# Performance work log

Hardware: AMD Instinct MI355X
Metric: run time of the kernel (lower is better)

The kernel has to match this reference:

```python
import jax, jax.numpy as jnp
import numpy as np

B, N, M, D = 8, 4096, 4096, 3


def setup_inputs() -> dict:
    key = jax.random.key(0)
    k1, k2 = jax.random.split(key)
    preds = jax.random.normal(k1, (B, M, D), dtype=jnp.float32)
    gts = jax.random.normal(k2, (B, N, D), dtype=jnp.float32)
    c = jnp.ones((1,), dtype=jnp.float32)
    return {"preds": preds, "gts": gts, "c": c}


def _huber(x, c):
    return jnp.where(x < c, 0.5 * x * x, c * x - 0.5 * c * c)


def reference(preds, gts, c):
    # P[b, i, j] = ||gts[b,i] - preds[b,j]||^2  (as in batch_pairwise_dist(gts, preds))
    rx = jnp.sum(gts * gts, axis=-1)              # [B, N]
    ry = jnp.sum(preds * preds, axis=-1)          # [B, M]
    zz = jnp.einsum('bnd,bmd->bnm', gts, preds)   # [B, N, M]
    P = rx[:, :, None] + ry[:, None, :] - 2.0 * zz
    mins1 = jnp.min(P, axis=1)                    # [B, M] min over gts
    mins2 = jnp.min(P, axis=2)                    # [B, N] min over preds
    loss = jnp.sum(_huber(mins1, c)) + jnp.sum(_huber(mins2, c))
    return loss
```

## Files before the change

kernel.cpp:

```cpp
#include <hip/hip_runtime.h>

typedef float v2f  __attribute__((ext_vector_type(2)));
typedef float v4f  __attribute__((ext_vector_type(4)));

#define NPTS   4096
#define NB     8
#define NZ     16
#define QPT    8
#define TPB    256
#define QPB    (TPB * QPT)
#define XB     (NPTS / QPB)
#define CHUNK  128
#define NGRP   (CHUNK / 4)
#define NCHUNK (NPTS / CHUNK)

__device__ __forceinline__ unsigned enc_f(float f) {
    unsigned u = __float_as_uint(f);
    return (u & 0x80000000u) ? ~u : (u | 0x80000000u);
}
__device__ __forceinline__ float dec_f(unsigned e) {
    unsigned u = (e & 0x80000000u) ? (e ^ 0x80000000u) : ~e;
    return __uint_as_float(u);
}

__device__ __forceinline__ v2f pk_fma(v2f a, v2f b, v2f c) {
    v2f d;
    asm("v_pk_fma_f32 %0, %1, %2, %3" : "=v"(d) : "v"(a), "v"(b), "v"(c));
    return d;
}
__device__ __forceinline__ v2f pk_mul(v2f a, v2f b) {
    v2f d;
    asm("v_pk_mul_f32 %0, %1, %2" : "=v"(d) : "v"(a), "v"(b));
    return d;
}
__device__ __forceinline__ float min3f(float a, float b, float c) {
    float d;
    asm("v_min3_f32 %0, %1, %2, %3" : "=v"(d) : "v"(a), "v"(b), "v"(c));
    return d;
}

__global__ __launch_bounds__(TPB, 2) void min_kernel(const float* __restrict__ preds,
                                                     const float* __restrict__ gts,
                                                     unsigned* __restrict__ mins) {
    const int z    = blockIdx.z;
    const int b    = z >> 1;
    const int pass = z & 1;
    const int tid  = threadIdx.x;

    const float* pts = pass ? preds : gts;
    const float* qrs = pass ? gts   : preds;

    __shared__ v4f SX[NGRP], SY[NGRP], SZ[NGRP];

    {
        const float* pb = pts + ((size_t)b * NPTS + blockIdx.y * CHUNK) * 3;
        if (tid < CHUNK) {
            ((float*)SX)[tid] = pb[tid * 3 + 0];
            ((float*)SY)[tid] = pb[tid * 3 + 1];
            ((float*)SZ)[tid] = pb[tid * 3 + 2];
        }
    }

    const float* qb    = qrs + (size_t)b * NPTS * 3;
    const int    jbase = blockIdx.x * QPB + tid;
    v2f   AX[QPT], AY[QPT], AZ[QPT];
    float R[QPT], acc[QPT];
#pragma unroll
    for (int q = 0; q < QPT; ++q) {
        int   j  = jbase + q * TPB;
        float qx = qb[j * 3 + 0];
        float qy = qb[j * 3 + 1];
        float qz = qb[j * 3 + 2];
        R[q]  = fmaf(qx, qx, fmaf(qy, qy, qz * qz));
        float ax = -2.0f * qx, ay = -2.0f * qy, az = -2.0f * qz;
        AX[q] = (v2f){ax, ax};
        AY[q] = (v2f){ay, ay};
        AZ[q] = (v2f){az, az};
        acc[q] = 3.4e38f;
    }
    __syncthreads();

#pragma unroll 2
    for (int g = 0; g < NGRP; ++g) {
        v4f X = SX[g], Y = SY[g], Z = SZ[g];
        v2f Xlo = X.lo, Xhi = X.hi;
        v2f Ylo = Y.lo, Yhi = Y.hi;
        v2f Zlo = Z.lo, Zhi = Z.hi;
        v2f Wlo = pk_fma(Xlo, Xlo, pk_fma(Ylo, Ylo, pk_mul(Zlo, Zlo)));
        v2f Whi = pk_fma(Xhi, Xhi, pk_fma(Yhi, Yhi, pk_mul(Zhi, Zhi)));
#pragma unroll
        for (int q = 0; q < QPT; ++q) {
            v2f t0 = pk_fma(Xlo, AX[q], pk_fma(Ylo, AY[q], pk_fma(Zlo, AZ[q], Wlo)));
            v2f t1 = pk_fma(Xhi, AX[q], pk_fma(Yhi, AY[q], pk_fma(Zhi, AZ[q], Whi)));
            acc[q] = min3f(t0.x, t0.y, min3f(t1.x, t1.y, acc[q]));
        }
    }

    unsigned* mz = mins + (size_t)z * NPTS;
#pragma unroll
    for (int q = 0; q < QPT; ++q) {
        atomicMin(&mz[jbase + q * TPB], enc_f(R[q] + acc[q]));
    }
}

__global__ __launch_bounds__(1024) void huberfinal_kernel(const unsigned* __restrict__ mins,
                                                          const float* __restrict__ cp,
                                                          float* __restrict__ out) {
    const float c = cp[0];
    float acc = 0.0f;
#pragma unroll 4
    for (int i = threadIdx.x; i < NZ * NPTS; i += 1024) {
        float x = dec_f(mins[i]);
        acc += (x < c) ? (0.5f * x * x) : fmaf(c, x, -0.5f * c * c);
    }
    for (int off = 32; off > 0; off >>= 1) acc += __shfl_down(acc, off, 64);
    __shared__ float ls[16];
    if ((threadIdx.x & 63) == 0) ls[threadIdx.x >> 6] = acc;
    __syncthreads();
    if (threadIdx.x == 0) {
        float s = 0.0f;
#pragma unroll
        for (int w = 0; w < 16; ++w) s += ls[w];
        out[0] = s;
    }
}

extern "C" void kernel_launch(void* const* d_in, const int* in_sizes, int n_in,
                              void* d_out, int out_size, void* d_ws, size_t ws_size,
                              hipStream_t stream) {
    const float* preds = (const float*)d_in[0];
    const float* gts   = (const float*)d_in[1];
    const float* cp    = (const float*)d_in[2];
    float* out = (float*)d_out;

    unsigned* mins = (unsigned*)d_ws;

    hipMemsetAsync(mins, 0xFF, (size_t)NZ * NPTS * sizeof(unsigned), stream);

    dim3 gm(XB, NCHUNK, NZ);
    min_kernel<<<gm, TPB, 0, stream>>>(preds, gts, mins);

    huberfinal_kernel<<<1, 1024, 0, stream>>>(mins, cp, out);
}
```

Before: 39.85 us.

## Replace atomicMin reduction with per-chunk partial stores and parallel Huber reduction

The min kernel now writes each chunk's per-query minimum to a partial buffer instead of doing encoded atomicMin, which removes the memset and atomic contention. A 256-block Huber kernel reduces the 32 partials per point and produces block sums, and a tiny final kernel sums those, replacing the single-block final pass. Launch bounds are raised to 4 blocks per SIMD. The cost is an extra 8 MB of partial writes and reads plus one more kernel launch.

```diff
diff --git a/kernel.cpp b/kernel.cpp
--- a/kernel.cpp
+++ b/kernel.cpp
@@ -4,7 +4,6 @@
 typedef float v4f  __attribute__((ext_vector_type(4)));
 
 #define NPTS   4096
-#define NB     8
 #define NZ     16
 #define QPT    8
 #define TPB    256
@@ -13,15 +12,6 @@
 #define CHUNK  128
 #define NGRP   (CHUNK / 4)
 #define NCHUNK (NPTS / CHUNK)
-
-__device__ __forceinline__ unsigned enc_f(float f) {
-    unsigned u = __float_as_uint(f);
-    return (u & 0x80000000u) ? ~u : (u | 0x80000000u);
-}
-__device__ __forceinline__ float dec_f(unsigned e) {
-    unsigned u = (e & 0x80000000u) ? (e ^ 0x80000000u) : ~e;
-    return __uint_as_float(u);
-}
 
 __device__ __forceinline__ v2f pk_fma(v2f a, v2f b, v2f c) {
     v2f d;
@@ -39,9 +29,9 @@
     return d;
 }
 
-__global__ __launch_bounds__(TPB, 2) void min_kernel(const float* __restrict__ preds,
+__global__ __launch_bounds__(TPB, 4) void min_kernel(const float* __restrict__ preds,
                                                      const float* __restrict__ gts,
-                                                     unsigned* __restrict__ mins) {
+                                                     float* __restrict__ partial) {
     const int z    = blockIdx.z;
     const int b    = z >> 1;
     const int pass = z & 1;
@@ -96,33 +86,39 @@
         }
     }
 
-    unsigned* mz = mins + (size_t)z * NPTS;
+    float* dst = partial + ((size_t)z * NCHUNK + blockIdx.y) * NPTS;
 #pragma unroll
     for (int q = 0; q < QPT; ++q) {
-        atomicMin(&mz[jbase + q * TPB], enc_f(R[q] + acc[q]));
+        dst[jbase + q * TPB] = R[q] + acc[q];
     }
 }
 
-__global__ __launch_bounds__(1024) void huberfinal_kernel(const unsigned* __restrict__ mins,
-                                                          const float* __restrict__ cp,
-                                                          float* __restrict__ out) {
-    const float c = cp[0];
-    float acc = 0.0f;
-#pragma unroll 4
-    for (int i = threadIdx.x; i < NZ * NPTS; i += 1024) {
-        float x = dec_f(mins[i]);
-        acc += (x < c) ? (0.5f * x * x) : fmaf(c, x, -0.5f * c * c);
-    }
-    for (int off = 32; off > 0; off >>= 1) acc += __shfl_down(acc, off, 64);
-    __shared__ float ls[16];
-    if ((threadIdx.x & 63) == 0) ls[threadIdx.x >> 6] = acc;
+__global__ __launch_bounds__(256) void huber_kernel(const float* __restrict__ partial,
+                                                    const float* __restrict__ cp,
+                                                    float* __restrict__ bp) {
+    const int s = blockIdx.x * 256 + threadIdx.x;
+    const int z = s >> 12, j = s & (NPTS - 1);
+    const float* p = partial + (size_t)z * NCHUNK * NPTS + j;
+    float m = 3.4e38f;
+#pragma unroll
+    for (int c = 0; c < NCHUNK; ++c) m = fminf(m, p[(size_t)c * NPTS]);
+    const float cc = cp[0];
+    float h = (m < cc) ? (0.5f * m * m) : fmaf(cc, m, -0.5f * cc * cc);
+    for (int off = 32; off > 0; off >>= 1) h += __shfl_down(h, off, 64);
+    __shared__ float ls[4];
+    if ((threadIdx.x & 63) == 0) ls[threadIdx.x >> 6] = h;
     __syncthreads();
-    if (threadIdx.x == 0) {
-        float s = 0.0f;
-#pragma unroll
-        for (int w = 0; w < 16; ++w) s += ls[w];
-        out[0] = s;
-    }
+    if (threadIdx.x == 0) bp[blockIdx.x] = ls[0] + ls[1] + ls[2] + ls[3];
+}
+
+__global__ __launch_bounds__(256) void final_kernel(const float* __restrict__ bp,
+                                                    float* __restrict__ out) {
+    float a = bp[threadIdx.x];
+    for (int off = 32; off > 0; off >>= 1) a += __shfl_down(a, off, 64);
+    __shared__ float ls[4];
+    if ((threadIdx.x & 63) == 0) ls[threadIdx.x >> 6] = a;
+    __syncthreads();
+    if (threadIdx.x == 0) out[0] = ls[0] + ls[1] + ls[2] + ls[3];
 }
 
 extern "C" void kernel_launch(void* const* d_in, const int* in_sizes, int n_in,
@@ -133,12 +129,12 @@
     const float* cp    = (const float*)d_in[2];
     float* out = (float*)d_out;
 
-    unsigned* mins = (unsigned*)d_ws;
-
-    hipMemsetAsync(mins, 0xFF, (size_t)NZ * NPTS * sizeof(unsigned), stream);
+    float* partial = (float*)d_ws;
+    float* bp      = partial + (size_t)NZ * NCHUNK * NPTS;
 
     dim3 gm(XB, NCHUNK, NZ);
-    min_kernel<<<gm, TPB, 0, stream>>>(preds, gts, mins);
+    min_kernel<<<gm, TPB, 0, stream>>>(preds, gts, partial);
 
-    huberfinal_kernel<<<1, 1024, 0, stream>>>(mins, cp, out);
+    huber_kernel<<<(NZ * NPTS) / 256, 256, 0, stream>>>(partial, cp, bp);
+    final_kernel<<<1, 256, 0, stream>>>(bp, out);
 }
```

Result: faster. 33.40 us (-16.2%).
